# Performance work log

Hardware: AMD Instinct MI355X
Metric: run time of the kernel (lower is better)

## Reference

```python
import jax, jax.numpy as jnp
import numpy as np


def setup_inputs() -> dict:
    key = jax.random.key(0)
    k1, k2 = jax.random.split(key)
    N, C, T, K = 8192, 3, 2048, 10
    Xt = jax.random.normal(k1, (N, C, T), dtype=jnp.float32)
    y_true = jax.random.randint(k2, (N,), 0, K, dtype=jnp.int64)
    return {"Xt": Xt, "y_true": y_true, "num_classes": K}


def reference(Xt, y_true, num_classes):
    # Within-Class Sum of Squares: for each class k,
    #   loss_k = mean((Xk - mean(Xk, axis=0))**2)  (mean over all elements)
    # total = mean over classes. Assumes all num_classes labels are present
    # (matches torch.unique iteration under this data distribution).
    N = Xt.shape[0]
    D = Xt.shape[1] * Xt.shape[2]  # elements per sample
    sums = jax.ops.segment_sum(Xt, y_true, num_segments=num_classes)        # [K, C, T]
    counts = jax.ops.segment_sum(jnp.ones((N,), Xt.dtype), y_true,
                                 num_segments=num_classes)                  # [K]
    means = sums / counts[:, None, None]                                    # [K, C, T]
    sq = jnp.square(Xt - means[y_true])                                     # [N, C, T]
    sq_per_sample = sq.reshape(N, -1).sum(axis=1)                           # [N]
    sq_sums = jax.ops.segment_sum(sq_per_sample, y_true,
                                  num_segments=num_classes)                 # [K]
    per_class_mse = sq_sums / (counts * D)                                  # [K]
    return per_class_mse.mean()
```

## Files before the change

kernel.cpp:

```cpp
#include <hip/hip_runtime.h>

#define N_SAMP 8192
#define D_DIM 6144
#define K_CLS 10
#define CHUNK 32
#define NCHUNKS (N_SAMP / CHUNK)
#define COLS_PER_BLOCK 1024
#define NGROUPS (D_DIM / COLS_PER_BLOCK)

__global__ __launch_bounds__(1024) void build_sort(const int* __restrict__ y,
                                                   int* __restrict__ counts,
                                                   int* __restrict__ sorted) {
    __shared__ int lcnt[K_CLS];
    __shared__ int loff[K_CLS];
    const int tid = threadIdx.x;
    if (tid < K_CLS) lcnt[tid] = 0;
    __syncthreads();
    for (int i = tid; i < N_SAMP; i += 1024) atomicAdd(&lcnt[y[i]], 1);
    __syncthreads();
    if (tid == 0) {
        int off = 0;
        for (int k = 0; k < K_CLS; ++k) {
            loff[k] = off; counts[k] = lcnt[k]; off += lcnt[k];
        }
    }
    __syncthreads();
    for (int i = tid; i < N_SAMP; i += 1024) {
        int pos = atomicAdd(&loff[y[i]], 1);
        sorted[pos] = i;
    }
}

__global__ __launch_bounds__(256) void wcss_accum(const float* __restrict__ X,
                                                  const int* __restrict__ y,
                                                  const int* __restrict__ sorted,
                                                  float* __restrict__ S1,
                                                  float* __restrict__ s2sum) {
    __shared__ int idx_lds[CHUNK];
    __shared__ int cls_lds[CHUNK];
    const int tid = threadIdx.x;
    const int col0 = blockIdx.x * COLS_PER_BLOCK + tid * 4;
    const int s0g = blockIdx.y * CHUNK;

    if (tid < CHUNK) {
        const int idx = sorted[s0g + tid];
        idx_lds[tid] = idx;
        cls_lds[tid] = y[idx];
    }
    __syncthreads();

    float4 a1 = make_float4(0.f, 0.f, 0.f, 0.f);
    float s2c = 0.f;
    int kcur = __builtin_amdgcn_readfirstlane(cls_lds[0]);

    float4 buf[4];
#pragma unroll
    for (int j = 0; j < 4; ++j)
        buf[j] = *(const float4*)(X + (size_t)idx_lds[j] * D_DIM + col0);

#pragma unroll 1
    for (int s0 = 0; s0 < CHUNK; s0 += 4) {
        float4 nbuf[4];
        const int np = (s0 + 4 < CHUNK) ? (s0 + 4) : (CHUNK - 4);
#pragma unroll
        for (int j = 0; j < 4; ++j)
            nbuf[j] = *(const float4*)(X + (size_t)idx_lds[np + j] * D_DIM + col0);

#pragma unroll
        for (int j = 0; j < 4; ++j) {
            const int yk = __builtin_amdgcn_readfirstlane(cls_lds[s0 + j]);
            if (yk != kcur) {
                float* b1 = S1 + kcur * D_DIM + col0;
                atomicAdd(b1 + 0, a1.x); atomicAdd(b1 + 1, a1.y);
                atomicAdd(b1 + 2, a1.z); atomicAdd(b1 + 3, a1.w);
                atomicAdd(&s2sum[kcur], s2c);
                a1 = make_float4(0.f, 0.f, 0.f, 0.f);
                s2c = 0.f;
                kcur = yk;
            }
            const float4 v = buf[j];
            a1.x += v.x; a1.y += v.y; a1.z += v.z; a1.w += v.w;
            s2c += v.x * v.x + v.y * v.y + v.z * v.z + v.w * v.w;
        }
#pragma unroll
        for (int j = 0; j < 4; ++j) buf[j] = nbuf[j];
    }

    float* b1 = S1 + kcur * D_DIM + col0;
    atomicAdd(b1 + 0, a1.x); atomicAdd(b1 + 1, a1.y);
    atomicAdd(b1 + 2, a1.z); atomicAdd(b1 + 3, a1.w);
    atomicAdd(&s2sum[kcur], s2c);
}

__global__ __launch_bounds__(256) void wcss_finish(const float* __restrict__ S1,
                                                   const float* __restrict__ s2sum,
                                                   const int* __restrict__ counts,
                                                   float* __restrict__ out) {
    __shared__ float sbuf[256];
    const int tid = threadIdx.x;
    const int k = blockIdx.x / NGROUPS;
    const int g = blockIdx.x % NGROUPS;
    const float cnt = (float)counts[k];
    const float inv = 1.0f / (cnt * cnt * (float)D_DIM * (float)K_CLS);

    const float4 v = *(const float4*)(S1 + k * D_DIM + g * COLS_PER_BLOCK + tid * 4);
    float t = -(v.x * v.x + v.y * v.y + v.z * v.z + v.w * v.w) * inv;
    if (g == 0 && tid == 0)
        t += s2sum[k] / (cnt * (float)D_DIM * (float)K_CLS);

    sbuf[tid] = t;
    __syncthreads();
    for (int off = 128; off > 0; off >>= 1) {
        if (tid < off) sbuf[tid] += sbuf[tid + off];
        __syncthreads();
    }
    if (tid == 0) atomicAdd(out, sbuf[0]);
}

extern "C" void kernel_launch(void* const* d_in, const int* in_sizes, int n_in,
                              void* d_out, int out_size, void* d_ws, size_t ws_size,
                              hipStream_t stream) {
    const float* X = (const float*)d_in[0];
    const int* y = (const int*)d_in[1];

    float* S1 = (float*)d_ws;
    float* s2sum = S1 + K_CLS * D_DIM;
    int* counts = (int*)(s2sum + K_CLS);
    int* sorted = counts + K_CLS;
    float* out = (float*)d_out;

    hipMemsetAsync(S1, 0, (K_CLS * D_DIM + K_CLS) * sizeof(float), stream);
    hipMemsetAsync(out, 0, sizeof(float), stream);

    build_sort<<<dim3(1), dim3(1024), 0, stream>>>(y, counts, sorted);
    wcss_accum<<<dim3(NGROUPS, NCHUNKS), dim3(256), 0, stream>>>(X, y, sorted, S1, s2sum);
    wcss_finish<<<dim3(K_CLS * NGROUPS), dim3(256), 0, stream>>>(S1, s2sum, counts, out);
}
```

Measured before the change: 347.2 us.

## Fuse zero-init into stable counting sort, pack class into index, deepen load pipeline

Removes the two memset launches by zeroing S1, s2sum and out inside the sort kernel. Replaces the atomic-based scatter with a stable per-thread histogram and prefix-scan counting sort. Packs the class label into the sorted index so the accumulation kernel skips the dependent y lookup. Widens the prefetch ring in the accumulation kernel from 4 to 8 loads in flight. The single-block sort now does serial zeroing of 61K floats, which may lengthen that stage.

```diff
diff --git a/kernel.cpp b/kernel.cpp
--- a/kernel.cpp
+++ b/kernel.cpp
@@ -7,32 +7,78 @@
 #define NCHUNKS (N_SAMP / CHUNK)
 #define COLS_PER_BLOCK 1024
 #define NGROUPS (D_DIM / COLS_PER_BLOCK)
+#define PIPE 8
 
-__global__ __launch_bounds__(1024) void build_sort(const int* __restrict__ y,
-                                                   int* __restrict__ counts,
-                                                   int* __restrict__ sorted) {
-    __shared__ int lcnt[K_CLS];
-    __shared__ int loff[K_CLS];
+__global__ __launch_bounds__(256) void build_sort(const int* __restrict__ y,
+                                                  int* __restrict__ counts,
+                                                  int* __restrict__ sorted,
+                                                  float* __restrict__ S1,
+                                                  float* __restrict__ s2sum,
+                                                  float* __restrict__ out) {
+    __shared__ int M[K_CLS * 256];
+    __shared__ int wsum[4];
     const int tid = threadIdx.x;
-    if (tid < K_CLS) lcnt[tid] = 0;
+    const int lane = tid & 63;
+    const int wid = tid >> 6;
+
+    for (int j = tid; j < K_CLS * D_DIM; j += 256) S1[j] = 0.0f;
+    if (tid < K_CLS) s2sum[tid] = 0.0f;
+    if (tid == 0) out[0] = 0.0f;
+
+    int h[K_CLS];
+#pragma unroll
+    for (int k = 0; k < K_CLS; ++k) h[k] = 0;
+    const int base = tid * 32;
+#pragma unroll 1
+    for (int i = 0; i < 32; ++i) {
+        const int yy = y[base + i];
+#pragma unroll
+        for (int k = 0; k < K_CLS; ++k) h[k] += (yy == k) ? 1 : 0;
+    }
+#pragma unroll
+    for (int k = 0; k < K_CLS; ++k) M[k * 256 + tid] = h[k];
     __syncthreads();
-    for (int i = tid; i < N_SAMP; i += 1024) atomicAdd(&lcnt[y[i]], 1);
+
+    int loc[10];
+    int run = 0;
+#pragma unroll
+    for (int j = 0; j < 10; ++j) { loc[j] = run; run += M[tid * 10 + j]; }
+    int v = run;
+#pragma unroll
+    for (int d = 1; d < 64; d <<= 1) {
+        int n = __shfl_up(v, d, 64);
+        if (lane >= d) v += n;
+    }
+    if (lane == 63) wsum[wid] = v;
     __syncthreads();
-    if (tid == 0) {
-        int off = 0;
-        for (int k = 0; k < K_CLS; ++k) {
-            loff[k] = off; counts[k] = lcnt[k]; off += lcnt[k];
-        }
+    int wbase = 0;
+#pragma unroll
+    for (int w = 0; w < 4; ++w) wbase += (w < wid) ? wsum[w] : 0;
+    const int tbase = wbase + (v - run);
+    __syncthreads();
+#pragma unroll
+    for (int j = 0; j < 10; ++j) M[tid * 10 + j] = tbase + loc[j];
+    __syncthreads();
+
+    if (tid < K_CLS) {
+        const int s = M[tid * 256];
+        const int e = (tid == K_CLS - 1) ? N_SAMP : M[(tid + 1) * 256];
+        counts[tid] = e - s;
     }
-    __syncthreads();
-    for (int i = tid; i < N_SAMP; i += 1024) {
-        int pos = atomicAdd(&loff[y[i]], 1);
-        sorted[pos] = i;
+
+    int off[K_CLS];
+#pragma unroll
+    for (int k = 0; k < K_CLS; ++k) off[k] = M[k * 256 + tid];
+#pragma unroll 1
+    for (int i = 0; i < 32; ++i) {
+        const int yy = y[base + i];
+#pragma unroll
+        for (int k = 0; k < K_CLS; ++k)
+            if (yy == k) sorted[off[k]++] = (k << 16) | (base + i);
     }
 }
 
 __global__ __launch_bounds__(256) void wcss_accum(const float* __restrict__ X,
-                                                  const int* __restrict__ y,
                                                   const int* __restrict__ sorted,
                                                   float* __restrict__ S1,
                                                   float* __restrict__ s2sum) {
@@ -43,47 +89,41 @@
     const int s0g = blockIdx.y * CHUNK;
 
     if (tid < CHUNK) {
-        const int idx = sorted[s0g + tid];
-        idx_lds[tid] = idx;
-        cls_lds[tid] = y[idx];
+        const int p = sorted[s0g + tid];
+        idx_lds[tid] = p & 0xffff;
+        cls_lds[tid] = p >> 16;
     }
     __syncthreads();
 
+    const float* base = X + col0;
     float4 a1 = make_float4(0.f, 0.f, 0.f, 0.f);
     float s2c = 0.f;
     int kcur = __builtin_amdgcn_readfirstlane(cls_lds[0]);
 
-    float4 buf[4];
+    float4 buf[PIPE];
 #pragma unroll
-    for (int j = 0; j < 4; ++j)
-        buf[j] = *(const float4*)(X + (size_t)idx_lds[j] * D_DIM + col0);
-
-#pragma unroll 1
-    for (int s0 = 0; s0 < CHUNK; s0 += 4) {
-        float4 nbuf[4];
-        const int np = (s0 + 4 < CHUNK) ? (s0 + 4) : (CHUNK - 4);
-#pragma unroll
-        for (int j = 0; j < 4; ++j)
-            nbuf[j] = *(const float4*)(X + (size_t)idx_lds[np + j] * D_DIM + col0);
+    for (int j = 0; j < PIPE; ++j)
+        buf[j] = *(const float4*)(base + (size_t)idx_lds[j] * D_DIM);
 
 #pragma unroll
-        for (int j = 0; j < 4; ++j) {
-            const int yk = __builtin_amdgcn_readfirstlane(cls_lds[s0 + j]);
-            if (yk != kcur) {
-                float* b1 = S1 + kcur * D_DIM + col0;
-                atomicAdd(b1 + 0, a1.x); atomicAdd(b1 + 1, a1.y);
-                atomicAdd(b1 + 2, a1.z); atomicAdd(b1 + 3, a1.w);
-                atomicAdd(&s2sum[kcur], s2c);
-                a1 = make_float4(0.f, 0.f, 0.f, 0.f);
-                s2c = 0.f;
-                kcur = yk;
-            }
-            const float4 v = buf[j];
-            a1.x += v.x; a1.y += v.y; a1.z += v.z; a1.w += v.w;
-            s2c += v.x * v.x + v.y * v.y + v.z * v.z + v.w * v.w;
+    for (int s = 0; s < CHUNK; ++s) {
+        const float4 v = buf[s & (PIPE - 1)];
+        if (s + PIPE < CHUNK)
+            buf[s & (PIPE - 1)] =
+                *(const float4*)(base + (size_t)idx_lds[s + PIPE] * D_DIM);
+
+        const int yk = __builtin_amdgcn_readfirstlane(cls_lds[s]);
+        if (yk != kcur) {
+            float* b1 = S1 + kcur * D_DIM + col0;
+            atomicAdd(b1 + 0, a1.x); atomicAdd(b1 + 1, a1.y);
+            atomicAdd(b1 + 2, a1.z); atomicAdd(b1 + 3, a1.w);
+            atomicAdd(&s2sum[kcur], s2c);
+            a1 = make_float4(0.f, 0.f, 0.f, 0.f);
+            s2c = 0.f;
+            kcur = yk;
         }
-#pragma unroll
-        for (int j = 0; j < 4; ++j) buf[j] = nbuf[j];
+        a1.x += v.x; a1.y += v.y; a1.z += v.z; a1.w += v.w;
+        s2c += v.x * v.x + v.y * v.y + v.z * v.z + v.w * v.w;
     }
 
     float* b1 = S1 + kcur * D_DIM + col0;
@@ -129,10 +169,7 @@
     int* sorted = counts + K_CLS;
     float* out = (float*)d_out;
 
-    hipMemsetAsync(S1, 0, (K_CLS * D_DIM + K_CLS) * sizeof(float), stream);
-    hipMemsetAsync(out, 0, sizeof(float), stream);
-
-    build_sort<<<dim3(1), dim3(1024), 0, stream>>>(y, counts, sorted);
-    wcss_accum<<<dim3(NGROUPS, NCHUNKS), dim3(256), 0, stream>>>(X, y, sorted, S1, s2sum);
+    build_sort<<<dim3(1), dim3(256), 0, stream>>>(y, counts, sorted, S1, s2sum, out);
+    wcss_accum<<<dim3(NGROUPS, NCHUNKS), dim3(256), 0, stream>>>(X, sorted, S1, s2sum);
     wcss_finish<<<dim3(K_CLS * NGROUPS), dim3(256), 0, stream>>>(S1, s2sum, counts, out);
 }
```

After: 352.4 us. About the same (+1.5%).
